# Kernel tuning notes

Hardware: AMD Instinct MI355X
Metric: run time of the kernel (lower is better)

## Reference

```python
import jax, jax.numpy as jnp
import numpy as np

B, T, C, HS = 8, 2048, 2048, 128  # batch, seq, n_embedding, head_size
THETA = 10000.0


def _rope_tables(dim, seq_len, theta=THETA):
    freqs = 1.0 / theta ** (jnp.arange(0, dim, 2, dtype=jnp.float32) / dim)  # [dim/2]
    t = jnp.arange(seq_len, dtype=jnp.float32)
    ang = jnp.outer(t, freqs)  # [T, dim/2]
    return jnp.cos(ang), jnp.sin(ang)


def _apply_rope(v, cos, sin):
    # v: [B,T,D]; pairs along last dim treated as complex (real=even, imag=odd)
    b, t, d = v.shape
    vr = v.reshape(b, t, d // 2, 2)
    x0, x1 = vr[..., 0], vr[..., 1]
    o0 = x0 * cos - x1 * sin
    o1 = x0 * sin + x1 * cos
    return jnp.stack([o0, o1], axis=-1).reshape(b, t, d)


def setup_inputs() -> dict:
    key = jax.random.key(0)
    k1, k2, k3, k4 = jax.random.split(key, 4)
    scale = 1.0 / np.sqrt(C)
    x = jax.random.normal(k1, (B, T, C), dtype=jnp.float32)
    Wk = jax.random.normal(k2, (C, HS), dtype=jnp.float32) * scale
    Wq = jax.random.normal(k3, (C, HS), dtype=jnp.float32) * scale
    Wv = jax.random.normal(k4, (C, HS), dtype=jnp.float32) * scale
    return {"x": x, "Wk": Wk, "Wq": Wq, "Wv": Wv}


def reference(x, Wk, Wq, Wv):
    b, t, _ = x.shape
    cos, sin = _rope_tables(HS, t)
    k = x @ Wk  # [B,T,HS]
    q = x @ Wq
    # Source: xq,xk = apply_rotary_emb(key, query); query,key = xq,xk
    # => scores = rope(q_proj) @ rope(k_proj)^T (standard causal attention)
    qr = _apply_rope(q, cos, sin)
    kr = _apply_rope(k, cos, sin)
    scores = jnp.einsum('btd,bsd->bts', qr, kr) * (HS ** -0.5)  # [B,T,T]
    causal = jnp.tril(jnp.ones((t, t), dtype=bool))
    scores = jnp.where(causal, scores, -jnp.inf)
    wei = jax.nn.softmax(scores, axis=-1)
    v = x @ Wv
    return jnp.einsum('bts,bsd->btd', wei, v)
```

## Files before the change

kernel.cpp:

```cpp
#include <hip/hip_runtime.h>

#define NB 8
#define NT 2048
#define NC 2048
#define NH 128

typedef short s8v __attribute__((ext_vector_type(8)));
typedef float f4  __attribute__((ext_vector_type(4)));

static __device__ __forceinline__ unsigned short f2bf(float f) {
    union { float f; unsigned int u; } v; v.f = f;
    unsigned int x = v.u;
    return (unsigned short)((x + 0x7FFFu + ((x >> 16) & 1u)) >> 16);
}

static __device__ __forceinline__ void gl2lds16(const void* g, void* lds_base) {
    __builtin_amdgcn_global_load_lds(
        (const __attribute__((address_space(1))) unsigned int*)g,
        (__attribute__((address_space(3))) unsigned int*)lds_base, 16, 0, 0);
}

__global__ __launch_bounds__(256) void wtrans_k(
    const float* __restrict__ Wk, const float* __restrict__ Wq,
    const float* __restrict__ Wv, unsigned short* __restrict__ wt)
{
    __shared__ float Ls[64][129];
    const int mat = blockIdx.y;
    const float* W = (mat == 0) ? Wq : (mat == 1) ? Wk : Wv;
    const int k0 = blockIdx.x * 64;
    const int t  = threadIdx.x;

    #pragma unroll
    for (int j = 0; j < 8; ++j) {
        int flat = j * 1024 + t * 4;
        int k = flat >> 7, n = flat & 127;
        f4 v = *reinterpret_cast<const f4*>(W + (size_t)(k0 + k) * NH + n);
        Ls[k][n] = v[0]; Ls[k][n + 1] = v[1]; Ls[k][n + 2] = v[2]; Ls[k][n + 3] = v[3];
    }
    __syncthreads();

    const int n = t >> 1, half = t & 1;
    unsigned short tmp[32];
    #pragma unroll
    for (int kk = 0; kk < 32; ++kk) tmp[kk] = f2bf(Ls[half * 32 + kk][n]);
    unsigned short* dst = wt + (size_t)mat * 262144 + (size_t)n * 2048 + k0 + half * 32;
    #pragma unroll
    for (int v = 0; v < 4; ++v)
        *reinterpret_cast<s8v*>(dst + v * 8) = *reinterpret_cast<s8v*>(tmp + v * 8);
}

__global__ __launch_bounds__(256) void proj_rope(
    const float* __restrict__ x, const unsigned short* __restrict__ wt,
    unsigned short* __restrict__ qws, unsigned short* __restrict__ kws,
    unsigned short* __restrict__ vtws)
{
    __shared__ char LDS[49152];
    char* AsB = LDS;
    char* BsB = LDS + 16384;

    const int mat  = blockIdx.y;
    const int tid  = threadIdx.x;
    const int wave = tid >> 6;
    const int lane = tid & 63;
    const int quad = lane >> 4, l16 = lane & 15;
    const int wm = wave >> 1, wn = wave & 1;
    const int M0 = blockIdx.x * 64;
    const unsigned short* wtm = wt + mat * (NH * NC);

    const float* asrc[8];
    unsigned int adst[8];
    #pragma unroll
    for (int s = 0; s < 8; ++s) {
        const int f   = tid + s * 256;
        const int row = f >> 5;
        const int kc  = (f & 31) * 4;
        asrc[s] = x + (size_t)(M0 + row) * NC + kc;
        const int c   = kc >> 3;
        const int pos = c ^ (row & 15);
        adst[s] = row * 256 + pos * 16 + (kc & 4) * 2;
    }

    const unsigned short* bsrc[8];
    #pragma unroll
    for (int s = 0; s < 8; ++s) {
        const int j   = wave * 8 + s;
        const int row = j * 4 + (lane >> 4);
        const int c   = (lane & 15) ^ (row & 15);
        bsrc[s] = wtm + (size_t)row * NC + c * 8;
    }

    f4 acc[2][4];
    #pragma unroll
    for (int mi = 0; mi < 2; ++mi)
        #pragma unroll
        for (int ni = 0; ni < 4; ++ni)
            acc[mi][ni] = (f4){0.f, 0.f, 0.f, 0.f};

    f4 areg[8];
    #pragma unroll
    for (int s = 0; s < 8; ++s)
        areg[s] = *reinterpret_cast<const f4*>(asrc[s]);

    for (int kk = 0; kk < NC; kk += 128) {
        #pragma unroll
        for (int s = 0; s < 8; ++s)
            gl2lds16(bsrc[s] + kk, BsB + (wave * 8 + s) * 1024);

        #pragma unroll
        for (int s = 0; s < 8; ++s) {
            union { f4 f; unsigned int u[4]; } v; v.f = areg[s];
            uint2 p;
            p.x = __builtin_amdgcn_perm(v.u[1], v.u[0], 0x07060302u);
            p.y = __builtin_amdgcn_perm(v.u[3], v.u[2], 0x07060302u);
            *reinterpret_cast<uint2*>(AsB + adst[s]) = p;
        }
        if (kk + 128 < NC) {
            #pragma unroll
            for (int s = 0; s < 8; ++s)
                areg[s] = *reinterpret_cast<const f4*>(asrc[s] + kk + 128);
        }
        __syncthreads();

        #pragma unroll
        for (int ksub = 0; ksub < 4; ++ksub) {
            const int c = ksub * 4 + quad;
            s8v a[2];
            #pragma unroll
            for (int mi = 0; mi < 2; ++mi) {
                const int row = wm * 32 + mi * 16 + l16;
                a[mi] = *reinterpret_cast<const s8v*>(AsB + row * 256 + (c ^ l16) * 16);
            }
            #pragma unroll
            for (int ni = 0; ni < 4; ++ni) {
                const int row2 = wn * 64 + ni * 16 + l16;
                s8v b = *reinterpret_cast<const s8v*>(BsB + row2 * 256 + (c ^ l16) * 16);
                acc[0][ni] = __builtin_amdgcn_mfma_f32_16x16x32_bf16(a[0], b, acc[0][ni], 0, 0, 0);
                acc[1][ni] = __builtin_amdgcn_mfma_f32_16x16x32_bf16(a[1], b, acc[1][ni], 0, 0, 0);
            }
        }
        __syncthreads();
    }

    const float cfreq = -0.10381025296f;
    #pragma unroll
    for (int mi = 0; mi < 2; ++mi) {
        #pragma unroll
        for (int ni = 0; ni < 4; ++ni) {
            const int col = wn * 64 + ni * 16 + l16;
            #pragma unroll
            for (int r = 0; r < 4; ++r) {
                const int row = M0 + wm * 32 + mi * 16 + quad * 4 + r;
                const int t   = row & (NT - 1);
                float v = acc[mi][ni][r];
                if (mat < 2) {
                    float other = __shfl_xor(v, 1, 64);
                    float freq  = exp2f(cfreq * (float)(col & ~1));
                    float ang   = (float)t * freq;
                    float sn = sinf(ang), cs = cosf(ang);
                    v = (col & 1) ? (other * sn + v * cs)
                                  : (v * cs - other * sn);
                }
                unsigned short bv = f2bf(v);
                if (mat == 0)      qws[(size_t)row * NH + col] = bv;
                else if (mat == 1) kws[(size_t)row * NH + col] = bv;
                else {
                    int b = row >> 11;
                    vtws[(size_t)b * (NH * NT) + (size_t)col * NT + t] = bv;
                }
            }
        }
    }
}

__global__ __launch_bounds__(256, 3) void attn_k(
    const unsigned short* __restrict__ qws, const unsigned short* __restrict__ kws,
    const unsigned short* __restrict__ vtws, float* __restrict__ out)
{
    __shared__ unsigned short P[4][16 * 64];
    __shared__ float Os[4][16][64];
    __shared__ float Ms[4][16], Ls[4][16], Lt[16];

    const int wave = threadIdx.x >> 6;
    const int lane = threadIdx.x & 63;
    const int quad = lane >> 4, l16 = lane & 15;
    const int b     = blockIdx.y;
    const int qrow0 = blockIdx.x * 16;
    const unsigned short* Q  = qws  + (size_t)b * NT * NH;
    const unsigned short* K  = kws  + (size_t)b * NT * NH;
    const unsigned short* Vt = vtws + (size_t)b * NH * NT;

    s8v qf[4];
    #pragma unroll
    for (int ks = 0; ks < 4; ++ks)
        qf[ks] = *reinterpret_cast<const s8v*>(
            Q + (size_t)(qrow0 + l16) * NH + ks * 32 + quad * 8);

    float m[4], ls[4];
    f4 o[8];
    #pragma unroll
    for (int r = 0; r < 4; ++r) { m[r] = -INFINITY; ls[r] = 0.f; }
    #pragma unroll
    for (int dt = 0; dt < 8; ++dt) o[dt] = (f4){0.f, 0.f, 0.f, 0.f};

    const int nkt = (qrow0 >> 6) + 1;
    const float scale = 0.0883883476f;

    for (int kt = wave; kt < nkt; kt += 4) {
        const int kbase = kt * 64;
        const bool domask = (kt == nkt - 1);

        f4 s[4];
        #pragma unroll
        for (int nt = 0; nt < 4; ++nt) {
            f4 a = (f4){0.f, 0.f, 0.f, 0.f};
            #pragma unroll
            for (int ks = 0; ks < 4; ++ks) {
                s8v kf = *reinterpret_cast<const s8v*>(
                    K + (size_t)(kbase + nt * 16 + l16) * NH + ks * 32 + quad * 8);
                a = __builtin_amdgcn_mfma_f32_16x16x32_bf16(qf[ks], kf, a, 0, 0, 0);
            }
            s[nt] = a;
        }

        #pragma unroll
        for (int r = 0; r < 4; ++r) {
            const int trow = qrow0 + quad * 4 + r;
            #pragma unroll
            for (int nt = 0; nt < 4; ++nt) {
                float sv = s[nt][r] * scale;
                if (domask && (kbase + nt * 16 + l16 > trow)) sv = -INFINITY;
                s[nt][r] = sv;
            }
            float tm = fmaxf(fmaxf(s[0][r], s[1][r]), fmaxf(s[2][r], s[3][r]));
            #pragma unroll
            for (int off = 1; off < 16; off <<= 1)
                tm = fmaxf(tm, __shfl_xor(tm, off, 64));
            const float mn = fmaxf(m[r], tm);
            const float alpha = __expf(m[r] - mn);
            m[r] = mn;
            float rs = 0.f;
            #pragma unroll
            for (int nt = 0; nt < 4; ++nt) {
                float p = __expf(s[nt][r] - mn);
                s[nt][r] = p;
                rs += p;
            }
            ls[r] = ls[r] * alpha + rs;
            #pragma unroll
            for (int dt = 0; dt < 8; ++dt) o[dt][r] *= alpha;
        }

        #pragma unroll
        for (int nt = 0; nt < 4; ++nt)
            #pragma unroll
            for (int r = 0; r < 4; ++r) {
                const int prow = quad * 4 + r;
                const int swz  = ((nt * 2 + (l16 >> 3)) ^ (prow & 7)) * 8 + (l16 & 7);
                P[wave][prow * 64 + swz] = f2bf(s[nt][r]);
            }

        #pragma unroll
        for (int ks2 = 0; ks2 < 2; ++ks2) {
            const int pp = (ks2 * 4 + quad) ^ (l16 & 7);
            s8v pa = *reinterpret_cast<const s8v*>(&P[wave][l16 * 64 + pp * 8]);
            #pragma unroll
            for (int dt = 0; dt < 8; ++dt) {
                s8v vf = *reinterpret_cast<const s8v*>(
                    Vt + (size_t)(dt * 16 + l16) * NT + kbase + ks2 * 32 + quad * 8);
                o[dt] = __builtin_amdgcn_mfma_f32_16x16x32_bf16(pa, vf, o[dt], 0, 0, 0);
            }
        }
    }

    #pragma unroll
    for (int r = 0; r < 4; ++r) {
        float v = ls[r];
        #pragma unroll
        for (int off = 1; off < 16; off <<= 1) v += __shfl_xor(v, off, 64);
        ls[r] = v;
    }

    if (l16 == 0) {
        #pragma unroll
        for (int r = 0; r < 4; ++r) {
            Ms[wave][quad * 4 + r] = m[r];
            Ls[wave][quad * 4 + r] = ls[r];
        }
    }
    __syncthreads();

    #pragma unroll
    for (int r = 0; r < 4; ++r) {
        const int row = quad * 4 + r;
        float M = fmaxf(fmaxf(Ms[0][row], Ms[1][row]), fmaxf(Ms[2][row], Ms[3][row]));
        float sc = __expf(m[r] - M);
        float lt = Ls[0][row] * __expf(Ms[0][row] - M) + Ls[1][row] * __expf(Ms[1][row] - M)
                 + Ls[2][row] * __expf(Ms[2][row] - M) + Ls[3][row] * __expf(Ms[3][row] - M);
        if (wave == 0 && l16 == 0) Lt[row] = lt;
        #pragma unroll
        for (int dt = 0; dt < 8; ++dt) o[dt][r] *= sc;
    }

    const int rrow = threadIdx.x >> 4;
    const int cx   = (threadIdx.x & 15) * 4;
    #pragma unroll
    for (int h = 0; h < 2; ++h) {
        __syncthreads();
        #pragma unroll
        for (int dtl = 0; dtl < 4; ++dtl)
            #pragma unroll
            for (int r = 0; r < 4; ++r)
                Os[wave][quad * 4 + r][dtl * 16 + l16] = o[h * 4 + dtl][r];
        __syncthreads();
        f4 sum = (f4){0.f, 0.f, 0.f, 0.f};
        #pragma unroll
        for (int w = 0; w < 4; ++w)
            sum += *reinterpret_cast<const f4*>(&Os[w][rrow][cx]);
        const float rl = 1.0f / Lt[rrow];
        *reinterpret_cast<f4*>(
            &out[((size_t)b * NT + qrow0 + rrow) * NH + h * 64 + cx]) = sum * rl;
    }
}

extern "C" void kernel_launch(void* const* d_in, const int* in_sizes, int n_in,
                              void* d_out, int out_size, void* d_ws, size_t ws_size,
                              hipStream_t stream) {
    const float* x  = (const float*)d_in[0];
    const float* Wk = (const float*)d_in[1];
    const float* Wq = (const float*)d_in[2];
    const float* Wv = (const float*)d_in[3];
    unsigned short* ws   = (unsigned short*)d_ws;
    unsigned short* wt   = ws;
    unsigned short* qws  = ws  + 786432;
    unsigned short* kws  = qws + 2097152;
    unsigned short* vtws = kws + 2097152;
    float* outp = (float*)d_out;

    wtrans_k<<<dim3(32, 3), 256, 0, stream>>>(Wk, Wq, Wv, wt);
    proj_rope<<<dim3(256, 3), 256, 0, stream>>>(x, wt, qws, kws, vtws);
    attn_k<<<dim3(128, 8), 256, 0, stream>>>(qws, kws, vtws, outp);
}
```

Baseline: 342.7 us.

## Load fp32 x directly to LDS and pair causal query tiles in 512-thread attention

```diff
diff --git a/kernel.cpp b/kernel.cpp
--- a/kernel.cpp
+++ b/kernel.cpp
@@ -54,39 +54,27 @@
     unsigned short* __restrict__ qws, unsigned short* __restrict__ kws,
     unsigned short* __restrict__ vtws)
 {
-    __shared__ char LDS[49152];
-    char* AsB = LDS;
+    __shared__ char LDS[32768];
+    char* XsB = LDS;
     char* BsB = LDS + 16384;
 
     const int mat  = blockIdx.y;
-    const int tid  = threadIdx.x;
-    const int wave = tid >> 6;
-    const int lane = tid & 63;
+    const int wave = threadIdx.x >> 6;
+    const int lane = threadIdx.x & 63;
     const int quad = lane >> 4, l16 = lane & 15;
     const int wm = wave >> 1, wn = wave & 1;
     const int M0 = blockIdx.x * 64;
     const unsigned short* wtm = wt + mat * (NH * NC);
 
-    const float* asrc[8];
-    unsigned int adst[8];
-    #pragma unroll
-    for (int s = 0; s < 8; ++s) {
-        const int f   = tid + s * 256;
-        const int row = f >> 5;
-        const int kc  = (f & 31) * 4;
-        asrc[s] = x + (size_t)(M0 + row) * NC + kc;
-        const int c   = kc >> 3;
-        const int pos = c ^ (row & 15);
-        adst[s] = row * 256 + pos * 16 + (kc & 4) * 2;
-    }
-
-    const unsigned short* bsrc[8];
-    #pragma unroll
-    for (int s = 0; s < 8; ++s) {
-        const int j   = wave * 8 + s;
-        const int row = j * 4 + (lane >> 4);
-        const int c   = (lane & 15) ^ (row & 15);
-        bsrc[s] = wtm + (size_t)row * NC + c * 8;
+    const float* xbase[4]; const unsigned short* bbase[4];
+    const int bc = (lane & 7) ^ (lane >> 3);
+    #pragma unroll
+    for (int s = 0; s < 4; ++s) {
+        const int xrow = wave * 16 + s * 4 + (lane >> 4);
+        const int xcol = ((lane & 15) ^ (xrow & 15)) * 4;
+        xbase[s] = x + (size_t)(M0 + xrow) * NC + xcol;
+        const int brow = wave * 32 + s * 8 + (lane >> 3);
+        bbase[s] = wtm + (size_t)brow * NC + bc * 8;
     }
 
     f4 acc[2][4];
@@ -96,44 +84,37 @@
         for (int ni = 0; ni < 4; ++ni)
             acc[mi][ni] = (f4){0.f, 0.f, 0.f, 0.f};
 
-    f4 areg[8];
-    #pragma unroll
-    for (int s = 0; s < 8; ++s)
-        areg[s] = *reinterpret_cast<const f4*>(asrc[s]);
-
-    for (int kk = 0; kk < NC; kk += 128) {
-        #pragma unroll
-        for (int s = 0; s < 8; ++s)
-            gl2lds16(bsrc[s] + kk, BsB + (wave * 8 + s) * 1024);
-
-        #pragma unroll
-        for (int s = 0; s < 8; ++s) {
-            union { f4 f; unsigned int u[4]; } v; v.f = areg[s];
-            uint2 p;
-            p.x = __builtin_amdgcn_perm(v.u[1], v.u[0], 0x07060302u);
-            p.y = __builtin_amdgcn_perm(v.u[3], v.u[2], 0x07060302u);
-            *reinterpret_cast<uint2*>(AsB + adst[s]) = p;
-        }
-        if (kk + 128 < NC) {
-            #pragma unroll
-            for (int s = 0; s < 8; ++s)
-                areg[s] = *reinterpret_cast<const f4*>(asrc[s] + kk + 128);
-        }
-        __syncthreads();
-
-        #pragma unroll
-        for (int ksub = 0; ksub < 4; ++ksub) {
-            const int c = ksub * 4 + quad;
+    for (int kk = 0; kk < NC; kk += 64) {
+        #pragma unroll
+        for (int s = 0; s < 4; ++s)
+            gl2lds16(xbase[s] + kk, XsB + (wave * 4 + s) * 1024);
+        #pragma unroll
+        for (int s = 0; s < 4; ++s)
+            gl2lds16(bbase[s] + kk, BsB + (wave * 4 + s) * 1024);
+        __syncthreads();
+
+        #pragma unroll
+        for (int ksub = 0; ksub < 2; ++ksub) {
             s8v a[2];
             #pragma unroll
             for (int mi = 0; mi < 2; ++mi) {
-                const int row = wm * 32 + mi * 16 + l16;
-                a[mi] = *reinterpret_cast<const s8v*>(AsB + row * 256 + (c ^ l16) * 16);
+                const int rb = (wm * 32 + mi * 16 + l16) * 256;
+                const int p0 = (ksub * 8 + quad * 2) ^ l16;
+                union { f4 f; unsigned int u[4]; } L, H;
+                L.f = *reinterpret_cast<const f4*>(XsB + rb + p0 * 16);
+                H.f = *reinterpret_cast<const f4*>(XsB + rb + (p0 ^ 1) * 16);
+                union { s8v s; unsigned int u[4]; } A;
+                A.u[0] = __builtin_amdgcn_perm(L.u[1], L.u[0], 0x07060302u);
+                A.u[1] = __builtin_amdgcn_perm(L.u[3], L.u[2], 0x07060302u);
+                A.u[2] = __builtin_amdgcn_perm(H.u[1], H.u[0], 0x07060302u);
+                A.u[3] = __builtin_amdgcn_perm(H.u[3], H.u[2], 0x07060302u);
+                a[mi] = A.s;
             }
             #pragma unroll
             for (int ni = 0; ni < 4; ++ni) {
                 const int row2 = wn * 64 + ni * 16 + l16;
-                s8v b = *reinterpret_cast<const s8v*>(BsB + row2 * 256 + (c ^ l16) * 16);
+                const int pb = (ksub * 4 + quad) ^ (l16 & 7);
+                s8v b = *reinterpret_cast<const s8v*>(BsB + row2 * 128 + pb * 16);
                 acc[0][ni] = __builtin_amdgcn_mfma_f32_16x16x32_bf16(a[0], b, acc[0][ni], 0, 0, 0);
                 acc[1][ni] = __builtin_amdgcn_mfma_f32_16x16x32_bf16(a[1], b, acc[1][ni], 0, 0, 0);
             }
@@ -172,153 +153,165 @@
     }
 }
 
-__global__ __launch_bounds__(256, 3) void attn_k(
+__global__ __launch_bounds__(512, 4) void attn_k(
     const unsigned short* __restrict__ qws, const unsigned short* __restrict__ kws,
     const unsigned short* __restrict__ vtws, float* __restrict__ out)
 {
-    __shared__ unsigned short P[4][16 * 64];
-    __shared__ float Os[4][16][64];
-    __shared__ float Ms[4][16], Ls[4][16], Lt[16];
-
-    const int wave = threadIdx.x >> 6;
-    const int lane = threadIdx.x & 63;
+    __shared__ unsigned short P[8][16 * 64];
+    __shared__ float Os[8][16][64];
+    __shared__ float Ms[8][16], Ls[8][16], Lt[16];
+
+    const int tid  = threadIdx.x;
+    const int wave = tid >> 6;
+    const int lane = tid & 63;
     const int quad = lane >> 4, l16 = lane & 15;
-    const int b     = blockIdx.y;
-    const int qrow0 = blockIdx.x * 16;
+    const int b    = blockIdx.y;
     const unsigned short* Q  = qws  + (size_t)b * NT * NH;
     const unsigned short* K  = kws  + (size_t)b * NT * NH;
     const unsigned short* Vt = vtws + (size_t)b * NH * NT;
-
-    s8v qf[4];
-    #pragma unroll
-    for (int ks = 0; ks < 4; ++ks)
-        qf[ks] = *reinterpret_cast<const s8v*>(
-            Q + (size_t)(qrow0 + l16) * NH + ks * 32 + quad * 8);
-
-    float m[4], ls[4];
-    f4 o[8];
-    #pragma unroll
-    for (int r = 0; r < 4; ++r) { m[r] = -INFINITY; ls[r] = 0.f; }
-    #pragma unroll
-    for (int dt = 0; dt < 8; ++dt) o[dt] = (f4){0.f, 0.f, 0.f, 0.f};
-
-    const int nkt = (qrow0 >> 6) + 1;
     const float scale = 0.0883883476f;
 
-    for (int kt = wave; kt < nkt; kt += 4) {
-        const int kbase = kt * 64;
-        const bool domask = (kt == nkt - 1);
-
-        f4 s[4];
-        #pragma unroll
-        for (int nt = 0; nt < 4; ++nt) {
-            f4 a = (f4){0.f, 0.f, 0.f, 0.f};
-            #pragma unroll
-            for (int ks = 0; ks < 4; ++ks) {
-                s8v kf = *reinterpret_cast<const s8v*>(
-                    K + (size_t)(kbase + nt * 16 + l16) * NH + ks * 32 + quad * 8);
-                a = __builtin_amdgcn_mfma_f32_16x16x32_bf16(qf[ks], kf, a, 0, 0, 0);
-            }
-            s[nt] = a;
+    #pragma unroll
+    for (int phase = 0; phase < 2; ++phase) {
+        const int qt    = phase == 0 ? (int)blockIdx.x : 127 - (int)blockIdx.x;
+        const int qrow0 = qt * 16;
+        const int nkt   = (qt >> 2) + 1;
+
+        s8v qf[4];
+        #pragma unroll
+        for (int ks = 0; ks < 4; ++ks)
+            qf[ks] = *reinterpret_cast<const s8v*>(
+                Q + (size_t)(qrow0 + l16) * NH + ks * 32 + quad * 8);
+
+        float m[4], ls[4];
+        f4 o[8];
+        #pragma unroll
+        for (int r = 0; r < 4; ++r) { m[r] = -INFINITY; ls[r] = 0.f; }
+        #pragma unroll
+        for (int dt = 0; dt < 8; ++dt) o[dt] = (f4){0.f, 0.f, 0.f, 0.f};
+
+        for (int kt = wave; kt < nkt; kt += 8) {
+            const int kbase = kt * 64;
+            const bool domask = (kt == nkt - 1);
+
+            f4 s[4];
+            #pragma unroll
+            for (int nt = 0; nt < 4; ++nt) {
+                f4 a = (f4){0.f, 0.f, 0.f, 0.f};
+                #pragma unroll
+                for (int ks = 0; ks < 4; ++ks) {
+                    s8v kf = *reinterpret_cast<const s8v*>(
+                        K + (size_t)(kbase + nt * 16 + l16) * NH + ks * 32 + quad * 8);
+                    a = __builtin_amdgcn_mfma_f32_16x16x32_bf16(qf[ks], kf, a, 0, 0, 0);
+                }
+                s[nt] = a;
+            }
+
+            #pragma unroll
+            for (int r = 0; r < 4; ++r) {
+                const int trow = qrow0 + quad * 4 + r;
+                #pragma unroll
+                for (int nt = 0; nt < 4; ++nt) {
+                    float sv = s[nt][r] * scale;
+                    if (domask && (kbase + nt * 16 + l16 > trow)) sv = -INFINITY;
+                    s[nt][r] = sv;
+                }
+                float tm = fmaxf(fmaxf(s[0][r], s[1][r]), fmaxf(s[2][r], s[3][r]));
+                #pragma unroll
+                for (int off = 1; off < 16; off <<= 1)
+                    tm = fmaxf(tm, __shfl_xor(tm, off, 64));
+                const float mn = fmaxf(m[r], tm);
+                const float alpha = __expf(m[r] - mn);
+                m[r] = mn;
+                float rs = 0.f;
+                #pragma unroll
+                for (int nt = 0; nt < 4; ++nt) {
+                    float p = __expf(s[nt][r] - mn);
+                    s[nt][r] = p;
+                    rs += p;
+                }
+                ls[r] = ls[r] * alpha + rs;
+                #pragma unroll
+                for (int dt = 0; dt < 8; ++dt) o[dt][r] *= alpha;
+            }
+
+            #pragma unroll
+            for (int nt = 0; nt < 4; ++nt)
+                #pragma unroll
+                for (int r = 0; r < 4; ++r) {
+                    const int prow = quad * 4 + r;
+                    const int swz  = ((nt * 2 + (l16 >> 3)) ^ (prow & 7)) * 8 + (l16 & 7);
+                    P[wave][prow * 64 + swz] = f2bf(s[nt][r]);
+                }
+
+            #pragma unroll
+            for (int ks2 = 0; ks2 < 2; ++ks2) {
+                const int pp = (ks2 * 4 + quad) ^ (l16 & 7);
+                s8v pa = *reinterpret_cast<const s8v*>(&P[wave][l16 * 64 + pp * 8]);
+                #pragma unroll
+                for (int dt = 0; dt < 8; ++dt) {
+                    s8v vf = *reinterpret_cast<const s8v*>(
+                        Vt + (size_t)(dt * 16 + l16) * NT + kbase + ks2 * 32 + quad * 8);
+                    o[dt] = __builtin_amdgcn_mfma_f32_16x16x32_bf16(pa, vf, o[dt], 0, 0, 0);
+                }
+            }
         }
 
         #pragma unroll
         for (int r = 0; r < 4; ++r) {
-            const int trow = qrow0 + quad * 4 + r;
-            #pragma unroll
-            for (int nt = 0; nt < 4; ++nt) {
-                float sv = s[nt][r] * scale;
-                if (domask && (kbase + nt * 16 + l16 > trow)) sv = -INFINITY;
-                s[nt][r] = sv;
-            }
-            float tm = fmaxf(fmaxf(s[0][r], s[1][r]), fmaxf(s[2][r], s[3][r]));
-            #pragma unroll
-            for (int off = 1; off < 16; off <<= 1)
-                tm = fmaxf(tm, __shfl_xor(tm, off, 64));
-            const float mn = fmaxf(m[r], tm);
-            const float alpha = __expf(m[r] - mn);
-            m[r] = mn;
-            float rs = 0.f;
-            #pragma unroll
-            for (int nt = 0; nt < 4; ++nt) {
-                float p = __expf(s[nt][r] - mn);
-                s[nt][r] = p;
-                rs += p;
-            }
-            ls[r] = ls[r] * alpha + rs;
-            #pragma unroll
-            for (int dt = 0; dt < 8; ++dt) o[dt][r] *= alpha;
-        }
-
-        #pragma unroll
-        for (int nt = 0; nt < 4; ++nt)
+            float v = ls[r];
+            #pragma unroll
+            for (int off = 1; off < 16; off <<= 1) v += __shfl_xor(v, off, 64);
+            ls[r] = v;
+        }
+
+        __syncthreads();
+        if (l16 == 0) {
             #pragma unroll
             for (int r = 0; r < 4; ++r) {
-                const int prow = quad * 4 + r;
-                const int swz  = ((nt * 2 + (l16 >> 3)) ^ (prow & 7)) * 8 + (l16 & 7);
-                P[wave][prow * 64 + swz] = f2bf(s[nt][r]);
-            }
-
-        #pragma unroll
-        for (int ks2 = 0; ks2 < 2; ++ks2) {
-            const int pp = (ks2 * 4 + quad) ^ (l16 & 7);
-            s8v pa = *reinterpret_cast<const s8v*>(&P[wave][l16 * 64 + pp * 8]);
-            #pragma unroll
-            for (int dt = 0; dt < 8; ++dt) {
-                s8v vf = *reinterpret_cast<const s8v*>(
-                    Vt + (size_t)(dt * 16 + l16) * NT + kbase + ks2 * 32 + quad * 8);
-                o[dt] = __builtin_amdgcn_mfma_f32_16x16x32_bf16(pa, vf, o[dt], 0, 0, 0);
-            }
-        }
-    }
-
-    #pragma unroll
-    for (int r = 0; r < 4; ++r) {
-        float v = ls[r];
-        #pragma unroll
-        for (int off = 1; off < 16; off <<= 1) v += __shfl_xor(v, off, 64);
-        ls[r] = v;
-    }
-
-    if (l16 == 0) {
+                Ms[wave][quad * 4 + r] = m[r];
+                Ls[wave][quad * 4 + r] = ls[r];
+            }
+        }
+        __syncthreads();
+
         #pragma unroll
         for (int r = 0; r < 4; ++r) {
-            Ms[wave][quad * 4 + r] = m[r];
-            Ls[wave][quad * 4 + r] = ls[r];
-        }
-    }
-    __syncthreads();
-
-    #pragma unroll
-    for (int r = 0; r < 4; ++r) {
-        const int row = quad * 4 + r;
-        float M = fmaxf(fmaxf(Ms[0][row], Ms[1][row]), fmaxf(Ms[2][row], Ms[3][row]));
-        float sc = __expf(m[r] - M);
-        float lt = Ls[0][row] * __expf(Ms[0][row] - M) + Ls[1][row] * __expf(Ms[1][row] - M)
-                 + Ls[2][row] * __expf(Ms[2][row] - M) + Ls[3][row] * __expf(Ms[3][row] - M);
-        if (wave == 0 && l16 == 0) Lt[row] = lt;
-        #pragma unroll
-        for (int dt = 0; dt < 8; ++dt) o[dt][r] *= sc;
-    }
-
-    const int rrow = threadIdx.x >> 4;
-    const int cx   = (threadIdx.x & 15) * 4;
-    #pragma unroll
-    for (int h = 0; h < 2; ++h) {
-        __syncthreads();
-        #pragma unroll
-        for (int dtl = 0; dtl < 4; ++dtl)
-            #pragma unroll
-            for (int r = 0; r < 4; ++r)
-                Os[wave][quad * 4 + r][dtl * 16 + l16] = o[h * 4 + dtl][r];
-        __syncthreads();
-        f4 sum = (f4){0.f, 0.f, 0.f, 0.f};
-        #pragma unroll
-        for (int w = 0; w < 4; ++w)
-            sum += *reinterpret_cast<const f4*>(&Os[w][rrow][cx]);
-        const float rl = 1.0f / Lt[rrow];
-        *reinterpret_cast<f4*>(
-            &out[((size_t)b * NT + qrow0 + rrow) * NH + h * 64 + cx]) = sum * rl;
+            const int row = quad * 4 + r;
+            float M = -INFINITY, lt = 0.f;
+            #pragma unroll
+            for (int w = 0; w < 8; ++w) M = fmaxf(M, Ms[w][row]);
+            #pragma unroll
+            for (int w = 0; w < 8; ++w) lt += Ls[w][row] * __expf(Ms[w][row] - M);
+            float sc = __expf(m[r] - M);
+            if (wave == 0 && l16 == 0) Lt[row] = lt;
+            #pragma unroll
+            for (int dt = 0; dt < 8; ++dt) o[dt][r] *= sc;
+        }
+
+        const int rrow = tid >> 5;
+        const int cf   = (tid & 31) * 2;
+        #pragma unroll
+        for (int h = 0; h < 2; ++h) {
+            __syncthreads();
+            #pragma unroll
+            for (int dtl = 0; dtl < 4; ++dtl)
+                #pragma unroll
+                for (int r = 0; r < 4; ++r)
+                    Os[wave][quad * 4 + r][dtl * 16 + l16] = o[h * 4 + dtl][r];
+            __syncthreads();
+            float s0 = 0.f, s1 = 0.f;
+            #pragma unroll
+            for (int w = 0; w < 8; ++w) {
+                s0 += Os[w][rrow][cf];
+                s1 += Os[w][rrow][cf + 1];
+            }
+            const float rl = 1.0f / Lt[rrow];
+            float2 res; res.x = s0 * rl; res.y = s1 * rl;
+            *reinterpret_cast<float2*>(
+                &out[((size_t)b * NT + qrow0 + rrow) * NH + h * 64 + cf]) = res;
+        }
+        __syncthreads();
     }
 }
 
@@ -338,5 +331,5 @@
 
     wtrans_k<<<dim3(32, 3), 256, 0, stream>>>(Wk, Wq, Wv, wt);
     proj_rope<<<dim3(256, 3), 256, 0, stream>>>(x, wt, qws, kws, vtws);
-    attn_k<<<dim3(128, 8), 256, 0, stream>>>(qws, kws, vtws, outp);
-}
+    attn_k<<<dim3(64, 8), 512, 0, stream>>>(qws, kws, vtws, outp);
+}
```

After: 326.7 us. 4.7% less time.
